# Kernel optimization log

Hardware: AMD Instinct MI355X
Metric: run time of the kernel (lower is better)

## Reference

```python
import jax, jax.numpy as jnp
import numpy as np

N_NODES = 100000
N_EDGES = 1600000
IN_DIM = 23
HID_DIM = 128
OUT_DIM = 64
NUM_GRAPHS = 64
EPS = 1e-12


def setup_inputs() -> dict:
    key = jax.random.key(0)
    ks = jax.random.split(key, 8)
    feat_0 = jax.random.normal(ks[0], (N_NODES, IN_DIM), dtype=jnp.float32)
    W1 = jax.random.normal(ks[1], (IN_DIM, HID_DIM), dtype=jnp.float32) * 0.1
    b1 = jax.random.normal(ks[2], (HID_DIM,), dtype=jnp.float32) * 0.1
    W2 = jax.random.normal(ks[3], (HID_DIM, OUT_DIM), dtype=jnp.float32) * 0.1
    b2 = jax.random.normal(ks[4], (OUT_DIM,), dtype=jnp.float32) * 0.1
    src = jax.random.randint(ks[5], (N_EDGES,), 0, N_NODES, dtype=jnp.int64 if jax.config.jax_enable_x64 else jnp.int32)
    dst = jax.random.randint(ks[6], (N_EDGES,), 0, N_NODES, dtype=src.dtype)
    graph_ids = jnp.sort(jax.random.randint(ks[7], (N_NODES,), 0, NUM_GRAPHS, dtype=src.dtype))
    return {"feat_0": feat_0, "W1": W1, "b1": b1, "W2": W2, "b2": b2,
            "src": src, "dst": dst, "graph_ids": graph_ids}


def _sage_gcn(h, src, dst, W, b):
    # DGL SAGEConv with aggregator_type='gcn':
    # h_neigh[v] = (sum_{u->v} h[u] + h[v]) / (in_deg(v) + 1); out = h_neigh @ W + b
    n = h.shape[0]
    agg = jax.ops.segment_sum(h[src], dst, num_segments=n)          # [N, d]
    deg = jax.ops.segment_sum(jnp.ones_like(dst, dtype=h.dtype), dst, num_segments=n)
    h_neigh = (agg + h) / (deg + 1.0)[:, None]
    return h_neigh @ W + b


def reference(feat_0, W1, b1, W2, b2, src, dst, graph_ids):
    # layer 1 + relu + L2 row-normalize (dropout omitted: eval mode)
    h = _sage_gcn(feat_0, src, dst, W1, b1)
    h = jax.nn.relu(h)
    norm = jnp.maximum(jnp.linalg.norm(h, axis=1, keepdims=True), EPS)
    h = h / norm
    # output layer
    h = _sage_gcn(h, src, dst, W2, b2)
    # dgl.mean_nodes: per-graph mean over nodes
    gsum = jax.ops.segment_sum(h, graph_ids, num_segments=NUM_GRAPHS)  # [G, out]
    cnt = jax.ops.segment_sum(jnp.ones((h.shape[0],), h.dtype), graph_ids, num_segments=NUM_GRAPHS)
    return gsum / jnp.maximum(cnt, 1.0)[:, None]
```

## Files before the change

### kernel.cpp

```cpp
#include <hip/hip_runtime.h>

#define IN_DIM 23
#define HID 128
#define OUTD 64
#define NGR 64
#define NXCD 8
#define FB_DIM 32
#define PH_STRIDE 136
#define A2_BLOCKS 2048
#define NB 256
#define CAP 8192
#define CHUNK 4096

typedef __attribute__((ext_vector_type(8))) short bf16x8;
typedef __attribute__((ext_vector_type(4))) float f32x4;
typedef __attribute__((ext_vector_type(2))) float f32x2;

static __device__ __forceinline__ unsigned xcd_id() {
    unsigned x;
    asm volatile("s_getreg_b32 %0, hwreg(20, 0, 32)" : "=s"(x));
    return x & (NXCD - 1);
}

static __device__ __forceinline__ unsigned short f2bf(float x) {
    unsigned u = __float_as_uint(x);
    unsigned r = (u + 0x7FFFu + ((u >> 16) & 1u)) >> 16;
    return (unsigned short)r;
}
static __device__ __forceinline__ float bf2f(unsigned short u) {
    return __uint_as_float((unsigned)u << 16);
}

static __device__ __forceinline__ unsigned enc_fp8(float x) {
    float a = fabsf(x);
    unsigned s = (__float_as_uint(x) >> 31) << 7;
    if (!(a > 0.f)) return s;
    a = fminf(a, 448.f);
    int eb; float fr = frexpf(a, &eb);
    int E = eb - 1;
    int code;
    if (E < -6) code = (int)rintf(ldexpf(a, 9));
    else        code = ((E + 7) << 3) + (int)rintf(ldexpf(fr, 4)) - 8;
    code = min(code, 0x7E);
    return s | (unsigned)code;
}

#if __has_builtin(__builtin_amdgcn_cvt_pk_f32_fp8)
static __device__ __forceinline__ void dec4_fp8(unsigned u, float& d0, float& d1,
                                                float& d2, float& d3) {
    f32x2 lo = __builtin_amdgcn_cvt_pk_f32_fp8((int)u, false);
    f32x2 hi = __builtin_amdgcn_cvt_pk_f32_fp8((int)u, true);
    d0 = lo[0]; d1 = lo[1]; d2 = hi[0]; d3 = hi[1];
}
#else
static __device__ __forceinline__ float dec1_fp8(unsigned b) {
    unsigned s = (b & 0x80u) << 24;
    unsigned em = b & 0x7Fu;
    float f = __uint_as_float(s | ((em << 20) + 0x3C000000u));
    if ((b & 0x78u) == 0)
        f = 2.f * f - __uint_as_float(s | 0x3C800000u);
    return f;
}
static __device__ __forceinline__ void dec4_fp8(unsigned u, float& d0, float& d1,
                                                float& d2, float& d3) {
    d0 = dec1_fp8(u & 0xFF); d1 = dec1_fp8((u >> 8) & 0xFF);
    d2 = dec1_fp8((u >> 16) & 0xFF); d3 = dec1_fp8(u >> 24);
}
#endif

__global__ __launch_bounds__(256) void k_featb(
    const float* __restrict__ feat0, unsigned short* __restrict__ featb,
    int n_nodes)
{
    int i = blockIdx.x * 256 + threadIdx.x;
    if (i >= n_nodes * FB_DIM) return;
    int v = i >> 5, d = i & (FB_DIM - 1);
    float x = (d < IN_DIM) ? feat0[(size_t)v * IN_DIM + d] : 0.f;
    featb[i] = f2bf(x);
}

__global__ __launch_bounds__(256) void k_wprep(
    const float* __restrict__ W1, const float* __restrict__ W2,
    unsigned short* __restrict__ W1t, unsigned short* __restrict__ W2t)
{
    int i = blockIdx.x * 256 + threadIdx.x;
    if (i < HID * 32) {
        int h = i >> 5, d = i & 31;
        W1t[i] = f2bf((d < IN_DIM) ? W1[d * HID + h] : 0.f);
    } else if (i < HID * 32 + OUTD * HID) {
        int j = i - HID * 32;
        int o = j >> 7, k = j & 127;
        W2t[j] = f2bf(W2[k * OUTD + o]);
    }
}

__global__ __launch_bounds__(256) void k_bin(
    const int* __restrict__ src, const int* __restrict__ dst,
    uint2* __restrict__ brec, int* __restrict__ bcur,
    int n_edges, int n_nodes)
{
    __shared__ int cnt[NB], offs[NB], cur[NB];
    __shared__ uint2 stage[CHUNK];
    int t = threadIdx.x;
    int e0 = blockIdx.x * CHUNK;
    int e1 = min(e0 + CHUNK, n_edges);
    cnt[t] = 0;
    __syncthreads();
    for (int e = e0 + t; e < e1; e += 256) {
        int b = (int)(((long long)dst[e] * NB) / n_nodes);
        atomicAdd(&cnt[b], 1);
    }
    __syncthreads();
    int c = cnt[t];
    offs[t] = c;
    __syncthreads();
    for (int off = 1; off < NB; off <<= 1) {
        int v = (t >= off) ? offs[t - off] : 0;
        __syncthreads();
        offs[t] += v;
        __syncthreads();
    }
    int excl = offs[t] - c;
    __syncthreads();
    offs[t] = excl;
    cur[t] = excl;
    __syncthreads();
    for (int e = e0 + t; e < e1; e += 256) {
        int u = src[e], v = dst[e];
        int b = (int)(((long long)v * NB) / n_nodes);
        int slot = atomicAdd(&cur[b], 1);
        stage[slot] = make_uint2((unsigned)u, (unsigned)v);
    }
    __syncthreads();
    int cc = cnt[t];
    int gb = 0;
    if (cc > 0) gb = atomicAdd(&bcur[t], cc);
    if (gb + cc > CAP) cc = max(0, CAP - gb);
    uint2* dp = brec + (size_t)t * CAP + gb;
    int sb = offs[t];
    for (int k = 0; k < cc; ++k) dp[k] = stage[sb + k];
}

__global__ __launch_bounds__(NB) void k_bscan(
    const int* __restrict__ bcur, int* __restrict__ bbase,
    int* __restrict__ rowstart, int n_nodes, int n_edges)
{
    __shared__ int s[NB];
    int t = threadIdx.x;
    int c = min(bcur[t], CAP);
    s[t] = c;
    __syncthreads();
    for (int off = 1; off < NB; off <<= 1) {
        int v = (t >= off) ? s[t - off] : 0;
        __syncthreads();
        s[t] += v;
        __syncthreads();
    }
    bbase[t] = s[t] - c;
    if (t == 0) rowstart[n_nodes] = n_edges;
}

__global__ __launch_bounds__(256) void k_csr(
    const uint2* __restrict__ brec, const int* __restrict__ bcur,
    const int* __restrict__ bbase, int* __restrict__ rowstart,
    int* __restrict__ eidx, int n_nodes)
{
    __shared__ int hist[512], scr[256];
    int b = blockIdx.x, t = threadIdx.x;
    int vlo = (int)(((long long)b * n_nodes + NB - 1) / NB);
    int vhi = (int)(((long long)(b + 1) * n_nodes + NB - 1) / NB);
    int nn = vhi - vlo;
    int bcnt = min(bcur[b], CAP);
    int base = bbase[b];
    for (int i = t; i < nn; i += 256) hist[i] = 0;
    __syncthreads();
    const uint2* rec = brec + (size_t)b * CAP;
    for (int r = t; r < bcnt; r += 256)
        atomicAdd(&hist[(int)rec[r].y - vlo], 1);
    __syncthreads();
    int i0 = 2 * t, i1 = i0 + 1;
    int a0 = (i0 < nn) ? hist[i0] : 0;
    int a1 = (i1 < nn) ? hist[i1] : 0;
    int s2 = a0 + a1;
    scr[t] = s2;
    __syncthreads();
    for (int off = 1; off < 256; off <<= 1) {
        int v = (t >= off) ? scr[t - off] : 0;
        __syncthreads();
        scr[t] += v;
        __syncthreads();
    }
    int excl = scr[t] - s2;
    __syncthreads();
    if (i0 < nn) hist[i0] = excl;
    if (i1 < nn) hist[i1] = excl + a0;
    __syncthreads();
    for (int i = t; i < nn; i += 256) rowstart[vlo + i] = base + hist[i];
    __syncthreads();
    for (int r = t; r < bcnt; r += 256) {
        uint2 e = rec[r];
        int pos = atomicAdd(&hist[(int)e.y - vlo], 1);
        eidx[base + pos] = (int)e.x;
    }
}

__global__ __launch_bounds__(256) void k_agg1(
    const int* __restrict__ rowstart, const int* __restrict__ eidx,
    const unsigned* __restrict__ fbd, const float* __restrict__ feat0,
    unsigned* __restrict__ hnbd, int n_nodes)
{
    int lane = threadIdx.x & 63;
    int quad = lane >> 4, l15 = lane & 15;
    int wglob = (int)((blockIdx.x * 256u + threadIdx.x) >> 6);
    int v = wglob * 4 + quad;
    if (v >= n_nodes) return;
    int e0 = rowstart[v], e1 = rowstart[v + 1];
    int nedge = e1 - e0;
    float a0 = 0.f, a1 = 0.f;
    for (int base = 0; base < nedge; base += 16) {
        int cnt = min(16, nedge - base);
        int idx = 0;
        if (l15 < cnt) idx = eidx[e0 + base + l15];
        unsigned uu[16];
#pragma unroll
        for (int j = 0; j < 16; ++j) {
            int s = __shfl(idx, quad * 16 + min(j, cnt - 1));
            uu[j] = 0u;
            if (j < cnt) uu[j] = fbd[(size_t)s * 16 + l15];
        }
#pragma unroll
        for (int j = 0; j < 16; ++j) {
            a0 += bf2f((unsigned short)(uu[j] & 0xFFFF));
            a1 += bf2f((unsigned short)(uu[j] >> 16));
        }
    }
    int d0 = 2 * l15, d1 = d0 + 1;
    float f0 = (d0 < IN_DIM) ? feat0[(size_t)v * IN_DIM + d0] : 0.f;
    float f1 = (d1 < IN_DIM) ? feat0[(size_t)v * IN_DIM + d1] : 0.f;
    float inv = 1.0f / ((float)nedge + 1.0f);
    unsigned out = (unsigned)f2bf((a0 + f0) * inv)
                 | ((unsigned)f2bf((a1 + f1) * inv) << 16);
    hnbd[(size_t)v * 16 + l15] = out;
}

__global__ __launch_bounds__(256) void k_node(
    const unsigned short* __restrict__ hnb, const unsigned short* __restrict__ W1t,
    const float* __restrict__ b1, const unsigned short* __restrict__ W2t,
    unsigned short* __restrict__ m1, int n_nodes)
{
    __shared__ unsigned short ph[4][16 * PH_STRIDE];
    int wave = threadIdx.x >> 6, lane = threadIdx.x & 63;
    int quad = lane >> 4, l15 = lane & 15;
    const f32x4 z4 = {0.f, 0.f, 0.f, 0.f};

    float bb[8];
#pragma unroll
    for (int t = 0; t < 8; ++t) bb[t] = b1[t * 16 + l15];

    for (int v0 = blockIdx.x * 64 + wave * 16; v0 < n_nodes; v0 += gridDim.x * 64) {
        bf16x8 aH = {0, 0, 0, 0, 0, 0, 0, 0};
        int vA = v0 + l15;
        if (vA < n_nodes) aH = *(const bf16x8*)&hnb[(size_t)vA * FB_DIM + quad * 8];
        f32x4 c1[8];
#pragma unroll
        for (int t = 0; t < 8; ++t) {
            bf16x8 bw = *(const bf16x8*)&W1t[(t * 16 + l15) * 32 + quad * 8];
            c1[t] = __builtin_amdgcn_mfma_f32_16x16x32_bf16(aH, bw, z4, 0, 0, 0);
        }
        float ssq[4] = {0.f, 0.f, 0.f, 0.f};
#pragma unroll
        for (int t = 0; t < 8; ++t) {
#pragma unroll
            for (int r = 0; r < 4; ++r) {
                float x = fmaxf(c1[t][r] + bb[t], 0.f);
                c1[t][r] = x;
                ssq[r] += x * x;
            }
        }
#pragma unroll
        for (int off = 1; off < 16; off <<= 1) {
#pragma unroll
            for (int r = 0; r < 4; ++r) ssq[r] += __shfl_xor(ssq[r], off);
        }
        float inv[4];
#pragma unroll
        for (int r = 0; r < 4; ++r) inv[r] = 1.0f / fmaxf(sqrtf(ssq[r]), 1e-12f);
#pragma unroll
        for (int t = 0; t < 8; ++t)
#pragma unroll
            for (int r = 0; r < 4; ++r)
                ph[wave][(quad * 4 + r) * PH_STRIDE + t * 16 + l15] =
                    f2bf(c1[t][r] * inv[r]);
        f32x4 c2[4] = {z4, z4, z4, z4};
#pragma unroll
        for (int ks = 0; ks < 4; ++ks) {
            bf16x8 aP = *(const bf16x8*)&ph[wave][l15 * PH_STRIDE + ks * 32 + quad * 8];
#pragma unroll
            for (int tn = 0; tn < 4; ++tn) {
                bf16x8 bw = *(const bf16x8*)&W2t[(tn * 16 + l15) * HID + ks * 32 + quad * 8];
                c2[tn] = __builtin_amdgcn_mfma_f32_16x16x32_bf16(aP, bw, c2[tn], 0, 0, 0);
            }
        }
#pragma unroll
        for (int tn = 0; tn < 4; ++tn)
#pragma unroll
            for (int r = 0; r < 4; ++r) {
                int v = v0 + quad * 4 + r;
                if (v < n_nodes) m1[(size_t)v * OUTD + tn * 16 + l15] = f2bf(c2[tn][r]);
            }
    }
}

__global__ __launch_bounds__(256) void k_m1f8(
    const unsigned short* __restrict__ m1b, unsigned* __restrict__ m1f8,
    int n_dwords)
{
    int i = blockIdx.x * 256 + threadIdx.x;
    if (i >= n_dwords) return;
    const unsigned short* p = &m1b[(size_t)i * 4];
    unsigned c = enc_fp8(bf2f(p[0])) | (enc_fp8(bf2f(p[1])) << 8)
               | (enc_fp8(bf2f(p[2])) << 16) | (enc_fp8(bf2f(p[3])) << 24);
    m1f8[i] = c;
}

__global__ __launch_bounds__(256) void k_agg2g(
    const int* __restrict__ rowstart, const int* __restrict__ eidx,
    const unsigned* __restrict__ md, const int* __restrict__ gids,
    float* __restrict__ gpart, int n_nodes)
{
    __shared__ float lsum[NGR * OUTD];
    int per = (n_nodes + (int)gridDim.x - 1) / (int)gridDim.x;
    int v_lo = blockIdx.x * per;
    int v_hi = min(v_lo + per, n_nodes);
    if (v_lo >= n_nodes) return;
    int g_lo = gids[v_lo], g_hi = gids[v_hi - 1];
    for (int i = g_lo * OUTD + threadIdx.x; i < (g_hi + 1) * OUTD; i += 256)
        lsum[i] = 0.f;
    __syncthreads();

    int lane = threadIdx.x & 63;
    int wave = threadIdx.x >> 6;
    int quad = lane >> 4, l15 = lane & 15;
    int curg = -1;
    float c0 = 0.f, c1 = 0.f, c2 = 0.f, c3 = 0.f;
    for (int v = v_lo + wave * 4 + quad; v < v_hi; v += 16) {
        int e0 = rowstart[v], e1 = rowstart[v + 1];
        int nedge = e1 - e0;
        float a0 = 0.f, a1 = 0.f, a2 = 0.f, a3 = 0.f;
        for (int base = 0; base < nedge; base += 16) {
            int cnt = min(16, nedge - base);
            int idx = 0;
            if (l15 < cnt) idx = eidx[e0 + base + l15];
            unsigned uu[16];
#pragma unroll
            for (int j = 0; j < 16; ++j) {
                int s = __shfl(idx, quad * 16 + min(j, cnt - 1));
                uu[j] = 0u;
                if (j < cnt) uu[j] = md[(size_t)s * 16 + l15];
            }
#pragma unroll
            for (int j = 0; j < 16; ++j) {
                float d0, d1, d2, d3;
                dec4_fp8(uu[j], d0, d1, d2, d3);
                a0 += d0; a1 += d1; a2 += d2; a3 += d3;
            }
        }
        {
            unsigned u = md[(size_t)v * 16 + l15];
            float d0, d1, d2, d3;
            dec4_fp8(u, d0, d1, d2, d3);
            a0 += d0; a1 += d1; a2 += d2; a3 += d3;
        }
        float inv = 1.0f / ((float)nedge + 1.0f);
        int g = gids[v];
        if (g != curg) {
            if (curg >= 0) {
                atomicAdd(&lsum[curg * OUTD + 4 * l15 + 0], c0);
                atomicAdd(&lsum[curg * OUTD + 4 * l15 + 1], c1);
                atomicAdd(&lsum[curg * OUTD + 4 * l15 + 2], c2);
                atomicAdd(&lsum[curg * OUTD + 4 * l15 + 3], c3);
            }
            curg = g;
            c0 = a0 * inv; c1 = a1 * inv; c2 = a2 * inv; c3 = a3 * inv;
        } else {
            c0 += a0 * inv; c1 += a1 * inv; c2 += a2 * inv; c3 += a3 * inv;
        }
    }
    if (curg >= 0) {
        atomicAdd(&lsum[curg * OUTD + 4 * l15 + 0], c0);
        atomicAdd(&lsum[curg * OUTD + 4 * l15 + 1], c1);
        atomicAdd(&lsum[curg * OUTD + 4 * l15 + 2], c2);
        atomicAdd(&lsum[curg * OUTD + 4 * l15 + 3], c3);
    }
    __syncthreads();
    float* gp = gpart + (size_t)xcd_id() * NGR * OUTD;
    for (int i = g_lo * OUTD + threadIdx.x; i < (g_hi + 1) * OUTD; i += 256)
        atomicAdd(&gp[i], lsum[i]);
}

__global__ void k_gcnt(const int* __restrict__ gids, float* __restrict__ gcnt,
                       int n_nodes)
{
    int g = threadIdx.x;
    if (g >= NGR) return;
    int lo = 0, hi = n_nodes;
    while (lo < hi) { int m = (lo + hi) >> 1; if (gids[m] < g) lo = m + 1; else hi = m; }
    int lb = lo;
    lo = 0; hi = n_nodes;
    while (lo < hi) { int m = (lo + hi) >> 1; if (gids[m] < g + 1) lo = m + 1; else hi = m; }
    gcnt[g] = (float)(lo - lb);
}

__global__ __launch_bounds__(256) void k_final(
    const float* __restrict__ gpart, const float* __restrict__ gcnt,
    const float* __restrict__ b2, float* __restrict__ out)
{
    int i = blockIdx.x * 256 + threadIdx.x;
    if (i >= NGR * OUTD) return;
    int g = i >> 6, d = i & 63;
    float s = 0.f;
#pragma unroll
    for (int p = 0; p < NXCD; ++p) s += gpart[(size_t)p * NGR * OUTD + i];
    float c = gcnt[g];
    out[i] = (c > 0.f) ? (s / c + b2[d]) : 0.f;
}

extern "C" void kernel_launch(void* const* d_in, const int* in_sizes, int n_in,
                              void* d_out, int out_size, void* d_ws, size_t ws_size,
                              hipStream_t stream) {
    const float* feat0 = (const float*)d_in[0];
    const float* W1    = (const float*)d_in[1];
    const float* b1    = (const float*)d_in[2];
    const float* W2    = (const float*)d_in[3];
    const float* b2    = (const float*)d_in[4];
    const int*   src   = (const int*)d_in[5];
    const int*   dst   = (const int*)d_in[6];
    const int*   gids  = (const int*)d_in[7];
    int n_edges = in_sizes[5];
    int n_nodes = in_sizes[7];

    unsigned short* W1t = (unsigned short*)d_ws;
    unsigned short* W2t = W1t + HID * 32;
    unsigned short* featb = W2t + (size_t)OUTD * HID;
    unsigned* m1f8 = (unsigned*)featb;
    char* up = (char*)(featb + (size_t)n_nodes * FB_DIM);
    up = (char*)(((uintptr_t)up + 15) & ~(uintptr_t)15);
    unsigned short* hnb = (unsigned short*)up;
    unsigned short* m1b = hnb + (size_t)n_nodes * FB_DIM;
    uint2* brec = (uint2*)up;
    size_t usz = (size_t)n_nodes * (FB_DIM + OUTD) * 2;
    size_t rsz = (size_t)NB * CAP * 8;
    char* after = up + (usz > rsz ? usz : rsz);
    after = (char*)(((uintptr_t)after + 15) & ~(uintptr_t)15);
    int*   eidx     = (int*)after;
    int*   rowstart = eidx + n_edges;
    int*   bcur     = rowstart + n_nodes + 1;
    int*   bbase    = bcur + NB;
    float* gpart    = (float*)(bbase + NB);
    float* gcnt     = gpart + (size_t)NXCD * NGR * OUTD;

    size_t zero_units = 2 * NB + (size_t)NXCD * NGR * OUTD + NGR;
    hipMemsetAsync(bcur, 0, zero_units * 4, stream);

    k_featb<<<(unsigned)(((long long)n_nodes * FB_DIM + 255) / 256), 256, 0, stream>>>(
        feat0, featb, n_nodes);
    k_wprep<<<(HID * 32 + OUTD * HID + 255) / 256, 256, 0, stream>>>(W1, W2, W1t, W2t);

    unsigned blkB = (unsigned)((n_edges + CHUNK - 1) / CHUNK);
    k_bin<<<blkB, 256, 0, stream>>>(src, dst, brec, bcur, n_edges, n_nodes);
    k_bscan<<<1, NB, 0, stream>>>(bcur, bbase, rowstart, n_nodes, n_edges);
    k_csr<<<NB, 256, 0, stream>>>(brec, bcur, bbase, rowstart, eidx, n_nodes);

    k_gcnt<<<1, 64, 0, stream>>>(gids, gcnt, n_nodes);

    unsigned blkA = (unsigned)((n_nodes + 15) / 16);
    k_agg1<<<blkA, 256, 0, stream>>>(rowstart, eidx, (const unsigned*)featb, feat0,
                                     (unsigned*)hnb, n_nodes);

    k_node<<<1024, 256, 0, stream>>>(hnb, W1t, b1, W2t, m1b, n_nodes);

    int n_dwords = n_nodes * 16;
    k_m1f8<<<(n_dwords + 255) / 256, 256, 0, stream>>>(m1b, m1f8, n_dwords);

    k_agg2g<<<A2_BLOCKS, 256, 0, stream>>>(rowstart, eidx, m1f8, gids, gpart,
                                           n_nodes);

    k_final<<<(NGR * OUTD + 255) / 256, 256, 0, stream>>>(gpart, gcnt, b2,
                                                          (float*)d_out);
}
```

Measured before the change: 235.8 us.

## Pack edge records, fuse fp8 encode into node kernel, merge small kernels

Binning now stores each edge as one 32-bit word: the source index plus the local destination offset in the high bits. It also reads src/dst only once, keeping them in registers between the count and scatter passes, which halves record traffic. The fp8 encoding moves into k_node using hardware pack-convert, so the separate k_m1f8 pass and its bf16 intermediate buffer are gone. k_gcnt is folded into k_bscan. agg1 reads the self term from the bf16 padded features instead of fp32 feat0, and agg2 changes the output column interleave to match the packed encode. Together these cut launches and memory traffic. The risks are that packing assumes node indices fit in 17 bits, the bf16 self feature slightly changes precision, and the int overflow checks on v*NB were removed.

```diff
diff --git a/kernel.cpp b/kernel.cpp
--- a/kernel.cpp
+++ b/kernel.cpp
@@ -45,12 +45,25 @@
     return s | (unsigned)code;
 }
 
+#if __has_builtin(__builtin_amdgcn_cvt_pk_fp8_f32)
+static __device__ __forceinline__ unsigned enc4_fp8(float a, float b,
+                                                    float c, float d) {
+    int r = __builtin_amdgcn_cvt_pk_fp8_f32(a, b, 0, false);
+    r = __builtin_amdgcn_cvt_pk_fp8_f32(c, d, r, true);
+    return (unsigned)r;
+}
+#else
+static __device__ __forceinline__ unsigned enc4_fp8(float a, float b,
+                                                    float c, float d) {
+    return enc_fp8(a) | (enc_fp8(b) << 8) | (enc_fp8(c) << 16)
+         | (enc_fp8(d) << 24);
+}
+#endif
+
 #if __has_builtin(__builtin_amdgcn_cvt_pk_f32_fp8)
-static __device__ __forceinline__ void dec4_fp8(unsigned u, float& d0, float& d1,
-                                                float& d2, float& d3) {
-    f32x2 lo = __builtin_amdgcn_cvt_pk_f32_fp8((int)u, false);
-    f32x2 hi = __builtin_amdgcn_cvt_pk_f32_fp8((int)u, true);
-    d0 = lo[0]; d1 = lo[1]; d2 = hi[0]; d3 = hi[1];
+static __device__ __forceinline__ void dec_pk(unsigned u, f32x2& lo, f32x2& hi) {
+    lo = __builtin_amdgcn_cvt_pk_f32_fp8((int)u, false);
+    hi = __builtin_amdgcn_cvt_pk_f32_fp8((int)u, true);
 }
 #else
 static __device__ __forceinline__ float dec1_fp8(unsigned b) {
@@ -61,10 +74,9 @@
         f = 2.f * f - __uint_as_float(s | 0x3C800000u);
     return f;
 }
-static __device__ __forceinline__ void dec4_fp8(unsigned u, float& d0, float& d1,
-                                                float& d2, float& d3) {
-    d0 = dec1_fp8(u & 0xFF); d1 = dec1_fp8((u >> 8) & 0xFF);
-    d2 = dec1_fp8((u >> 16) & 0xFF); d3 = dec1_fp8(u >> 24);
+static __device__ __forceinline__ void dec_pk(unsigned u, f32x2& lo, f32x2& hi) {
+    lo[0] = dec1_fp8(u & 0xFF);        lo[1] = dec1_fp8((u >> 8) & 0xFF);
+    hi[0] = dec1_fp8((u >> 16) & 0xFF); hi[1] = dec1_fp8(u >> 24);
 }
 #endif
 
@@ -96,19 +108,30 @@
 
 __global__ __launch_bounds__(256) void k_bin(
     const int* __restrict__ src, const int* __restrict__ dst,
-    uint2* __restrict__ brec, int* __restrict__ bcur,
+    unsigned* __restrict__ brec, int* __restrict__ bcur,
     int n_edges, int n_nodes)
 {
     __shared__ int cnt[NB], offs[NB], cur[NB];
-    __shared__ uint2 stage[CHUNK];
+    __shared__ unsigned stage[CHUNK];
     int t = threadIdx.x;
     int e0 = blockIdx.x * CHUNK;
     int e1 = min(e0 + CHUNK, n_edges);
+    int myb[16];
+    unsigned myrec[16];
     cnt[t] = 0;
     __syncthreads();
-    for (int e = e0 + t; e < e1; e += 256) {
-        int b = (int)(((long long)dst[e] * NB) / n_nodes);
-        atomicAdd(&cnt[b], 1);
+#pragma unroll
+    for (int k = 0; k < 16; ++k) {
+        int e = e0 + k * 256 + t;
+        myb[k] = -1;
+        if (e < e1) {
+            int u = src[e], v = dst[e];
+            int b = (v * NB) / n_nodes;
+            int vlo = (b * n_nodes + NB - 1) / NB;
+            myb[k] = b;
+            myrec[k] = (unsigned)u | ((unsigned)(v - vlo) << 17);
+            atomicAdd(&cnt[b], 1);
+        }
     }
     __syncthreads();
     int c = cnt[t];
@@ -125,25 +148,27 @@
     offs[t] = excl;
     cur[t] = excl;
     __syncthreads();
-    for (int e = e0 + t; e < e1; e += 256) {
-        int u = src[e], v = dst[e];
-        int b = (int)(((long long)v * NB) / n_nodes);
-        int slot = atomicAdd(&cur[b], 1);
-        stage[slot] = make_uint2((unsigned)u, (unsigned)v);
+#pragma unroll
+    for (int k = 0; k < 16; ++k) {
+        if (myb[k] >= 0) {
+            int slot = atomicAdd(&cur[myb[k]], 1);
+            stage[slot] = myrec[k];
+        }
     }
     __syncthreads();
     int cc = cnt[t];
     int gb = 0;
     if (cc > 0) gb = atomicAdd(&bcur[t], cc);
     if (gb + cc > CAP) cc = max(0, CAP - gb);
-    uint2* dp = brec + (size_t)t * CAP + gb;
+    unsigned* dp = brec + (size_t)t * CAP + gb;
     int sb = offs[t];
     for (int k = 0; k < cc; ++k) dp[k] = stage[sb + k];
 }
 
 __global__ __launch_bounds__(NB) void k_bscan(
     const int* __restrict__ bcur, int* __restrict__ bbase,
-    int* __restrict__ rowstart, int n_nodes, int n_edges)
+    int* __restrict__ rowstart, const int* __restrict__ gids,
+    float* __restrict__ gcnt, int n_nodes, int n_edges)
 {
     __shared__ int s[NB];
     int t = threadIdx.x;
@@ -158,25 +183,34 @@
     }
     bbase[t] = s[t] - c;
     if (t == 0) rowstart[n_nodes] = n_edges;
+    if (t < NGR) {
+        int g = t;
+        int lo = 0, hi = n_nodes;
+        while (lo < hi) { int m = (lo + hi) >> 1; if (gids[m] < g) lo = m + 1; else hi = m; }
+        int lb = lo;
+        lo = 0; hi = n_nodes;
+        while (lo < hi) { int m = (lo + hi) >> 1; if (gids[m] < g + 1) lo = m + 1; else hi = m; }
+        gcnt[g] = (float)(lo - lb);
+    }
 }
 
 __global__ __launch_bounds__(256) void k_csr(
-    const uint2* __restrict__ brec, const int* __restrict__ bcur,
+    const unsigned* __restrict__ brec, const int* __restrict__ bcur,
     const int* __restrict__ bbase, int* __restrict__ rowstart,
     int* __restrict__ eidx, int n_nodes)
 {
     __shared__ int hist[512], scr[256];
     int b = blockIdx.x, t = threadIdx.x;
-    int vlo = (int)(((long long)b * n_nodes + NB - 1) / NB);
-    int vhi = (int)(((long long)(b + 1) * n_nodes + NB - 1) / NB);
+    int vlo = (b * n_nodes + NB - 1) / NB;
+    int vhi = ((b + 1) * n_nodes + NB - 1) / NB;
     int nn = vhi - vlo;
     int bcnt = min(bcur[b], CAP);
     int base = bbase[b];
     for (int i = t; i < nn; i += 256) hist[i] = 0;
     __syncthreads();
-    const uint2* rec = brec + (size_t)b * CAP;
+    const unsigned* rec = brec + (size_t)b * CAP;
     for (int r = t; r < bcnt; r += 256)
-        atomicAdd(&hist[(int)rec[r].y - vlo], 1);
+        atomicAdd(&hist[rec[r] >> 17], 1);
     __syncthreads();
     int i0 = 2 * t, i1 = i0 + 1;
     int a0 = (i0 < nn) ? hist[i0] : 0;
@@ -198,16 +232,15 @@
     for (int i = t; i < nn; i += 256) rowstart[vlo + i] = base + hist[i];
     __syncthreads();
     for (int r = t; r < bcnt; r += 256) {
-        uint2 e = rec[r];
-        int pos = atomicAdd(&hist[(int)e.y - vlo], 1);
-        eidx[base + pos] = (int)e.x;
+        unsigned e = rec[r];
+        int pos = atomicAdd(&hist[e >> 17], 1);
+        eidx[base + pos] = (int)(e & 0x1FFFFu);
     }
 }
 
 __global__ __launch_bounds__(256) void k_agg1(
     const int* __restrict__ rowstart, const int* __restrict__ eidx,
-    const unsigned* __restrict__ fbd, const float* __restrict__ feat0,
-    unsigned* __restrict__ hnbd, int n_nodes)
+    const unsigned* __restrict__ fbd, unsigned* __restrict__ hnbd, int n_nodes)
 {
     int lane = threadIdx.x & 63;
     int quad = lane >> 4, l15 = lane & 15;
@@ -234,19 +267,17 @@
             a1 += bf2f((unsigned short)(uu[j] >> 16));
         }
     }
-    int d0 = 2 * l15, d1 = d0 + 1;
-    float f0 = (d0 < IN_DIM) ? feat0[(size_t)v * IN_DIM + d0] : 0.f;
-    float f1 = (d1 < IN_DIM) ? feat0[(size_t)v * IN_DIM + d1] : 0.f;
+    unsigned su = fbd[(size_t)v * 16 + l15];
     float inv = 1.0f / ((float)nedge + 1.0f);
-    unsigned out = (unsigned)f2bf((a0 + f0) * inv)
-                 | ((unsigned)f2bf((a1 + f1) * inv) << 16);
-    hnbd[(size_t)v * 16 + l15] = out;
+    float r0 = (a0 + bf2f((unsigned short)(su & 0xFFFF))) * inv;
+    float r1 = (a1 + bf2f((unsigned short)(su >> 16))) * inv;
+    hnbd[(size_t)v * 16 + l15] = (unsigned)f2bf(r0) | ((unsigned)f2bf(r1) << 16);
 }
 
 __global__ __launch_bounds__(256) void k_node(
     const unsigned short* __restrict__ hnb, const unsigned short* __restrict__ W1t,
     const float* __restrict__ b1, const unsigned short* __restrict__ W2t,
-    unsigned short* __restrict__ m1, int n_nodes)
+    unsigned* __restrict__ m1f8, int n_nodes)
 {
     __shared__ unsigned short ph[4][16 * PH_STRIDE];
     int wave = threadIdx.x >> 6, lane = threadIdx.x & 63;
@@ -302,25 +333,14 @@
             }
         }
 #pragma unroll
-        for (int tn = 0; tn < 4; ++tn)
-#pragma unroll
-            for (int r = 0; r < 4; ++r) {
-                int v = v0 + quad * 4 + r;
-                if (v < n_nodes) m1[(size_t)v * OUTD + tn * 16 + l15] = f2bf(c2[tn][r]);
-            }
-    }
-}
-
-__global__ __launch_bounds__(256) void k_m1f8(
-    const unsigned short* __restrict__ m1b, unsigned* __restrict__ m1f8,
-    int n_dwords)
-{
-    int i = blockIdx.x * 256 + threadIdx.x;
-    if (i >= n_dwords) return;
-    const unsigned short* p = &m1b[(size_t)i * 4];
-    unsigned c = enc_fp8(bf2f(p[0])) | (enc_fp8(bf2f(p[1])) << 8)
-               | (enc_fp8(bf2f(p[2])) << 16) | (enc_fp8(bf2f(p[3])) << 24);
-    m1f8[i] = c;
+        for (int r = 0; r < 4; ++r) {
+            int v = v0 + quad * 4 + r;
+            if (v < n_nodes) {
+                unsigned pk = enc4_fp8(c2[0][r], c2[1][r], c2[2][r], c2[3][r]);
+                m1f8[(size_t)v * 16 + l15] = pk;
+            }
+        }
+    }
 }
 
 __global__ __launch_bounds__(256) void k_agg2g(
@@ -342,11 +362,11 @@
     int wave = threadIdx.x >> 6;
     int quad = lane >> 4, l15 = lane & 15;
     int curg = -1;
-    float c0 = 0.f, c1 = 0.f, c2 = 0.f, c3 = 0.f;
+    f32x2 c01 = {0.f, 0.f}, c23 = {0.f, 0.f};
     for (int v = v_lo + wave * 4 + quad; v < v_hi; v += 16) {
         int e0 = rowstart[v], e1 = rowstart[v + 1];
         int nedge = e1 - e0;
-        float a0 = 0.f, a1 = 0.f, a2 = 0.f, a3 = 0.f;
+        f32x2 a01 = {0.f, 0.f}, a23 = {0.f, 0.f};
         for (int base = 0; base < nedge; base += 16) {
             int cnt = min(16, nedge - base);
             int idx = 0;
@@ -360,55 +380,43 @@
             }
 #pragma unroll
             for (int j = 0; j < 16; ++j) {
-                float d0, d1, d2, d3;
-                dec4_fp8(uu[j], d0, d1, d2, d3);
-                a0 += d0; a1 += d1; a2 += d2; a3 += d3;
+                f32x2 lo, hi;
+                dec_pk(uu[j], lo, hi);
+                a01 += lo; a23 += hi;
             }
         }
         {
-            unsigned u = md[(size_t)v * 16 + l15];
-            float d0, d1, d2, d3;
-            dec4_fp8(u, d0, d1, d2, d3);
-            a0 += d0; a1 += d1; a2 += d2; a3 += d3;
+            f32x2 lo, hi;
+            dec_pk(md[(size_t)v * 16 + l15], lo, hi);
+            a01 += lo; a23 += hi;
         }
         float inv = 1.0f / ((float)nedge + 1.0f);
         int g = gids[v];
         if (g != curg) {
             if (curg >= 0) {
-                atomicAdd(&lsum[curg * OUTD + 4 * l15 + 0], c0);
-                atomicAdd(&lsum[curg * OUTD + 4 * l15 + 1], c1);
-                atomicAdd(&lsum[curg * OUTD + 4 * l15 + 2], c2);
-                atomicAdd(&lsum[curg * OUTD + 4 * l15 + 3], c3);
+                atomicAdd(&lsum[curg * OUTD + l15 +  0], c01[0]);
+                atomicAdd(&lsum[curg * OUTD + l15 + 16], c01[1]);
+                atomicAdd(&lsum[curg * OUTD + l15 + 32], c23[0]);
+                atomicAdd(&lsum[curg * OUTD + l15 + 48], c23[1]);
             }
             curg = g;
-            c0 = a0 * inv; c1 = a1 * inv; c2 = a2 * inv; c3 = a3 * inv;
+            c01[0] = a01[0] * inv; c01[1] = a01[1] * inv;
+            c23[0] = a23[0] * inv; c23[1] = a23[1] * inv;
         } else {
-            c0 += a0 * inv; c1 += a1 * inv; c2 += a2 * inv; c3 += a3 * inv;
+            c01[0] += a01[0] * inv; c01[1] += a01[1] * inv;
+            c23[0] += a23[0] * inv; c23[1] += a23[1] * inv;
         }
     }
     if (curg >= 0) {
-        atomicAdd(&lsum[curg * OUTD + 4 * l15 + 0], c0);
-        atomicAdd(&lsum[curg * OUTD + 4 * l15 + 1], c1);
-        atomicAdd(&lsum[curg * OUTD + 4 * l15 + 2], c2);
-        atomicAdd(&lsum[curg * OUTD + 4 * l15 + 3], c3);
+        atomicAdd(&lsum[curg * OUTD + l15 +  0], c01[0]);
+        atomicAdd(&lsum[curg * OUTD + l15 + 16], c01[1]);
+        atomicAdd(&lsum[curg * OUTD + l15 + 32], c23[0]);
+        atomicAdd(&lsum[curg * OUTD + l15 + 48], c23[1]);
     }
     __syncthreads();
     float* gp = gpart + (size_t)xcd_id() * NGR * OUTD;
     for (int i = g_lo * OUTD + threadIdx.x; i < (g_hi + 1) * OUTD; i += 256)
         atomicAdd(&gp[i], lsum[i]);
-}
-
-__global__ void k_gcnt(const int* __restrict__ gids, float* __restrict__ gcnt,
-                       int n_nodes)
-{
-    int g = threadIdx.x;
-    if (g >= NGR) return;
-    int lo = 0, hi = n_nodes;
-    while (lo < hi) { int m = (lo + hi) >> 1; if (gids[m] < g) lo = m + 1; else hi = m; }
-    int lb = lo;
-    lo = 0; hi = n_nodes;
-    while (lo < hi) { int m = (lo + hi) >> 1; if (gids[m] < g + 1) lo = m + 1; else hi = m; }
-    gcnt[g] = (float)(lo - lb);
 }
 
 __global__ __launch_bounds__(256) void k_final(
@@ -446,10 +454,9 @@
     char* up = (char*)(featb + (size_t)n_nodes * FB_DIM);
     up = (char*)(((uintptr_t)up + 15) & ~(uintptr_t)15);
     unsigned short* hnb = (unsigned short*)up;
-    unsigned short* m1b = hnb + (size_t)n_nodes * FB_DIM;
-    uint2* brec = (uint2*)up;
-    size_t usz = (size_t)n_nodes * (FB_DIM + OUTD) * 2;
-    size_t rsz = (size_t)NB * CAP * 8;
+    unsigned* brec = (unsigned*)up;
+    size_t usz = (size_t)n_nodes * FB_DIM * 2;
+    size_t rsz = (size_t)NB * CAP * 4;
     char* after = up + (usz > rsz ? usz : rsz);
     after = (char*)(((uintptr_t)after + 15) & ~(uintptr_t)15);
     int*   eidx     = (int*)after;
@@ -468,19 +475,15 @@
 
     unsigned blkB = (unsigned)((n_edges + CHUNK - 1) / CHUNK);
     k_bin<<<blkB, 256, 0, stream>>>(src, dst, brec, bcur, n_edges, n_nodes);
-    k_bscan<<<1, NB, 0, stream>>>(bcur, bbase, rowstart, n_nodes, n_edges);
+    k_bscan<<<1, NB, 0, stream>>>(bcur, bbase, rowstart, gids, gcnt,
+                                  n_nodes, n_edges);
     k_csr<<<NB, 256, 0, stream>>>(brec, bcur, bbase, rowstart, eidx, n_nodes);
 
-    k_gcnt<<<1, 64, 0, stream>>>(gids, gcnt, n_nodes);
-
     unsigned blkA = (unsigned)((n_nodes + 15) / 16);
-    k_agg1<<<blkA, 256, 0, stream>>>(rowstart, eidx, (const unsigned*)featb, feat0,
+    k_agg1<<<blkA, 256, 0, stream>>>(rowstart, eidx, (const unsigned*)featb,
                                      (unsigned*)hnb, n_nodes);
 
-    k_node<<<1024, 256, 0, stream>>>(hnb, W1t, b1, W2t, m1b, n_nodes);
-
-    int n_dwords = n_nodes * 16;
-    k_m1f8<<<(n_dwords + 255) / 256, 256, 0, stream>>>(m1b, m1f8, n_dwords);
+    k_node<<<1024, 256, 0, stream>>>(hnb, W1t, b1, W2t, m1f8, n_nodes);
 
     k_agg2g<<<A2_BLOCKS, 256, 0, stream>>>(rowstart, eidx, m1f8, gids, gpart,
                                            n_nodes);
```

Measured after the change: 224.3 us. -4.9%, faster.
